# Kernel optimization log

Hardware: AMD Instinct MI355X
Metric: run time of the kernel (lower is better)

## Reference

```python
import jax, jax.numpy as jnp
import numpy as np

NUM_USER = 300000
NUM_ITEM = 200000
N = NUM_USER + NUM_ITEM
NNZ = 10000000
D = 64


def setup_inputs() -> dict:
    key = jax.random.key(0)
    k1, k2, k3, k4, k5, k6 = jax.random.split(key, 6)
    users_emb = jax.random.normal(k1, (NUM_USER, D), dtype=jnp.float32)
    items_emb = jax.random.normal(k2, (NUM_ITEM, D), dtype=jnp.float32)
    graph_vals = jax.random.uniform(k3, (NNZ,), dtype=jnp.float32)
    w = jax.random.normal(k4, (D, D), dtype=jnp.float32) * 0.1
    graph_rows = jax.random.randint(k5, (NNZ,), 0, N, dtype=jnp.int32)
    graph_cols = jax.random.randint(k6, (NNZ,), 0, N, dtype=jnp.int32)
    return {
        "users_emb": users_emb,
        "items_emb": items_emb,
        "graph_vals": graph_vals,
        "w": w,
        "graph_rows": graph_rows,
        "graph_cols": graph_cols,
    }


def reference(users_emb, items_emb, graph_vals, w, graph_rows, graph_cols):
    num_user = users_emb.shape[0]
    all_emb = jnp.concatenate([users_emb, items_emb], axis=0)  # [N, D]
    # sparse.mm(graph, all_emb): gather source rows, scale by edge value, scatter-add to dest rows
    msgs = graph_vals[:, None] * all_emb[graph_cols]  # [nnz, D]
    agg = jax.ops.segment_sum(msgs, graph_rows, num_segments=all_emb.shape[0])  # [N, D]
    out = agg @ w                      # non_linear dense transform
    out = jax.nn.leaky_relu(out, negative_slope=0.2)  # activation
    h_u2 = out[:num_user]
    h_i2 = out[num_user:]
    return (h_u2, h_i2)
```

## Files before the change

kernel.cpp:

```cpp
#include <hip/hip_runtime.h>
#include <hip/hip_bf16.h>

#define NUM_USER 300000
#define NUM_ITEM 200000
#define NTOT (NUM_USER + NUM_ITEM)
#define D 64
#define RPB 128
#define NB ((NTOT + RPB - 1) / RPB)
#define NBLK 256
#define ASTR 65
#define AW 8


__global__ __launch_bounds__(256) void hist_bucket(
    const int* __restrict__ rows, int* __restrict__ blockhist, int nnz)
{
    __shared__ int h[NB];
    for (int i = threadIdx.x; i < NB; i += 256) h[i] = 0;
    __syncthreads();
    int chunk = (nnz + NBLK - 1) / NBLK;
    int lo = blockIdx.x * chunk;
    int hi = min(lo + chunk, nnz);
    for (int e = lo + threadIdx.x; e < hi; e += 256)
        atomicAdd(&h[__builtin_nontemporal_load(&rows[e]) >> 7], 1);
    __syncthreads();
    for (int i = threadIdx.x; i < NB; i += 256)
        blockhist[blockIdx.x * NB + i] = h[i];
}


__global__ __launch_bounds__(256) void colscan(
    int* __restrict__ blockhist, int* __restrict__ coltotal)
{
    int kb = blockIdx.x * 256 + threadIdx.x;
    if (kb >= NB) return;
    int sum = 0;
    for (int b = 0; b < NBLK; b++) {
        int v = blockhist[b * NB + kb];
        blockhist[b * NB + kb] = sum;
        sum += v;
    }
    coltotal[kb] = sum;
}


__global__ __launch_bounds__(256) void bucketscan(
    const int* __restrict__ coltotal, int* __restrict__ bucketbase, int nnz)
{
    __shared__ int s[256];
    int t = threadIdx.x;
    int local[16];
    int sum = 0;
    #pragma unroll
    for (int i = 0; i < 16; i++) {
        int idx = t * 16 + i;
        int c = (idx < NB) ? coltotal[idx] : 0;
        local[i] = sum;
        sum += c;
    }
    s[t] = sum;
    __syncthreads();
    int v = sum;
    for (int off = 1; off < 256; off <<= 1) {
        int add = (t >= off) ? s[t - off] : 0;
        __syncthreads();
        s[t] += add;
        __syncthreads();
    }
    int base = s[t] - v;
    #pragma unroll
    for (int i = 0; i < 16; i++) {
        int idx = t * 16 + i;
        if (idx < NB) bucketbase[idx] = base + local[i];
    }
    if (t == 255) bucketbase[NB] = base + sum;
}


template<bool FAST>
__global__ __launch_bounds__(256) void scatter_bucket(
    const int* __restrict__ rows, const int* __restrict__ cols,
    const float* __restrict__ vals,
    const int* __restrict__ blockhist, const int* __restrict__ bucketbase,
    int* __restrict__ order, int2* __restrict__ rec2, int nnz)
{
    __shared__ int cur[NB];
    for (int i = threadIdx.x; i < NB; i += 256)
        cur[i] = blockhist[blockIdx.x * NB + i] + bucketbase[i];
    __syncthreads();
    int chunk = (nnz + NBLK - 1) / NBLK;
    int lo = blockIdx.x * chunk;
    int hi = min(lo + chunk, nnz);
    for (int e = lo + threadIdx.x; e < hi; e += 256) {
        int r = __builtin_nontemporal_load(&rows[e]);
        int pos = atomicAdd(&cur[r >> 7], 1);
        if (FAST) {
            int   c = __builtin_nontemporal_load(&cols[e]);
            float v = __builtin_nontemporal_load(&vals[e]);
            rec2[pos] = make_int2(((r & (RPB - 1)) << 19) | c,
                                  __float_as_int(v));
        } else {
            order[pos] = ((r & (RPB - 1)) << 24) | e;
        }
    }
}


__global__ __launch_bounds__(256) void rescatter2(
    const long long* __restrict__ rec2, const int* __restrict__ bucketbase,
    int* __restrict__ rowptr, long long* __restrict__ rec3)
{
    __shared__ int cnt[RPB];
    __shared__ int cur[RPB];
    __shared__ int s[256];
    int t = threadIdx.x;
    int kb = blockIdx.x;
    int row0 = kb * RPB;
    int start = bucketbase[kb], end = bucketbase[kb + 1];

    if (t < RPB) cnt[t] = 0;
    __syncthreads();
    for (int i = start + t; i < end; i += 256) {
        int key = (int)(rec2[i] & 0xffffffffLL);
        atomicAdd(&cnt[(key >> 19) & (RPB - 1)], 1);
    }
    __syncthreads();
    int v = (t < RPB) ? cnt[t] : 0;
    s[t] = v;
    __syncthreads();
    for (int off = 1; off < 256; off <<= 1) {
        int add = (t >= off) ? s[t - off] : 0;
        __syncthreads();
        s[t] += add;
        __syncthreads();
    }
    if (t < RPB) {
        int excl = s[t] - v;
        int p = start + excl;
        cur[t] = p;
        if (row0 + t <= NTOT) rowptr[row0 + t] = p;
    }
    __syncthreads();
    for (int i = start + t; i < end; i += 256) {
        long long rc = rec2[i];
        int key = (int)(rc & 0xffffffffLL);
        int lr  = (key >> 19) & (RPB - 1);
        int pos = atomicAdd(&cur[lr], 1);
        long long outrec = (rc & 0xffffffff00000000LL)
                         | (unsigned int)(key & 0x7FFFF);
        rec3[pos] = outrec;
    }
}


__global__ __launch_bounds__(256) void gather_rows(
    const float* __restrict__ users_emb, const float* __restrict__ items_emb,
    const long long* __restrict__ rec3, const int* __restrict__ rowptr,
    float* __restrict__ out, int n)
{
    int r = blockIdx.x * 4 + (threadIdx.x >> 6);
    if (r >= n) return;
    int lane = threadIdx.x & 63;
    int sub  = lane >> 4;
    int qi   = lane & 15;
    int k0 = rowptr[r];
    int k1 = rowptr[r + 1];
    float4 a0 = make_float4(0.f, 0.f, 0.f, 0.f);
    float4 a1 = make_float4(0.f, 0.f, 0.f, 0.f);
    #pragma unroll 2
    for (int g = k0; g < k1; g += 8) {
        int ka = g + sub;
        int kb = g + 4 + sub;
        long long rca = __builtin_nontemporal_load(&rec3[ka < k1 ? ka : k1 - 1]);
        long long rcb = __builtin_nontemporal_load(&rec3[kb < k1 ? kb : k1 - 1]);
        int   ca = (int)(rca & 0x7FFFFLL);
        int   cb = (int)(rcb & 0x7FFFFLL);
        float va = (ka < k1) ? __int_as_float((int)(rca >> 32)) : 0.f;
        float vb = (kb < k1) ? __int_as_float((int)(rcb >> 32)) : 0.f;
        const float* sa = (ca < NUM_USER)
            ? users_emb + (size_t)ca * D
            : items_emb + (size_t)(ca - NUM_USER) * D;
        const float* sb = (cb < NUM_USER)
            ? users_emb + (size_t)cb * D
            : items_emb + (size_t)(cb - NUM_USER) * D;
        float4 ea = *(const float4*)(sa + (qi << 2));
        float4 eb = *(const float4*)(sb + (qi << 2));
        a0.x = fmaf(va, ea.x, a0.x); a0.y = fmaf(va, ea.y, a0.y);
        a0.z = fmaf(va, ea.z, a0.z); a0.w = fmaf(va, ea.w, a0.w);
        a1.x = fmaf(vb, eb.x, a1.x); a1.y = fmaf(vb, eb.y, a1.y);
        a1.z = fmaf(vb, eb.z, a1.z); a1.w = fmaf(vb, eb.w, a1.w);
    }
    float4 a;
    a.x = a0.x + a1.x; a.y = a0.y + a1.y;
    a.z = a0.z + a1.z; a.w = a0.w + a1.w;
    a.x += __shfl_xor(a.x, 16); a.y += __shfl_xor(a.y, 16);
    a.z += __shfl_xor(a.z, 16); a.w += __shfl_xor(a.w, 16);
    a.x += __shfl_xor(a.x, 32); a.y += __shfl_xor(a.y, 32);
    a.z += __shfl_xor(a.z, 32); a.w += __shfl_xor(a.w, 32);
    if (sub == 0)
        *(float4*)(out + (size_t)r * D + (qi << 2)) = a;
}


template<bool FAST>
__global__ __launch_bounds__(512) void accum_kernel(
    const float* __restrict__ users_emb, const float* __restrict__ items_emb,
    const float* __restrict__ vals, const int* __restrict__ cols,
    const long long* __restrict__ rec2, const int* __restrict__ order,
    const int* __restrict__ bucketbase, float* __restrict__ out)
{
    __shared__ float acc[RPB * ASTR];
    int tid = threadIdx.x;
    for (int i = tid; i < RPB * ASTR; i += 512) acc[i] = 0.f;
    __syncthreads();

    int kb = blockIdx.x;
    int start = bucketbase[kb];
    int end   = bucketbase[kb + 1];
    int lane = tid & 63;
    int wid  = tid >> 6;
    int sub  = lane >> 4;
    int qi   = lane & 15;

    int span = end - start;
    int T = (span + (AW * 4 - 1)) / (AW * 4);
    int e0 = start + wid * 4 + sub;

    for (int it = 0; it < T; it++) {
        int e  = e0 + it * (AW * 4);
        int ec = max(start, min(e, end - 1));
        int ck; float v;
        if (FAST) {
            long long rc = __builtin_nontemporal_load(&rec2[ec]);
            ck = (int)(rc & 0xffffffffLL);
            v  = (e < end) ? __int_as_float((int)(rc >> 32)) : 0.f;
        } else {
            int rec  = __builtin_nontemporal_load(&order[ec]);
            int eid  = rec & 0xFFFFFF;
            int lrow = rec >> 24;
            ck = __builtin_nontemporal_load(&cols[eid]) | (lrow << 19);
            v  = (e < end) ? __builtin_nontemporal_load(&vals[eid]) : 0.f;
        }
        int cj = ck & 0x7FFFF;
        int lr = (ck >> 19) & (RPB - 1);
        const float* src = (cj < NUM_USER)
            ? users_emb + (size_t)cj * D
            : items_emb + (size_t)(cj - NUM_USER) * D;
        float4 e4 = *(const float4*)(src + (qi << 2));
        int ab = lr * ASTR + (qi << 2);
        atomicAdd(&acc[ab + 0], v * e4.x);
        atomicAdd(&acc[ab + 1], v * e4.y);
        atomicAdd(&acc[ab + 2], v * e4.z);
        atomicAdd(&acc[ab + 3], v * e4.w);
    }
    __syncthreads();

    size_t row0 = (size_t)kb * RPB;
    float4* o4 = (float4*)(out + row0 * D);
    for (int i = tid; i < RPB * (D / 4); i += 512) {
        int row = i >> 4, c4 = (i & 15) << 2;
        size_t grow = row0 + row;
        if (grow < NTOT) {
            float4 o;
            o.x = acc[row * ASTR + c4 + 0];
            o.y = acc[row * ASTR + c4 + 1];
            o.z = acc[row * ASTR + c4 + 2];
            o.w = acc[row * ASTR + c4 + 3];
            o4[i] = o;
        }
    }
}


__global__ __launch_bounds__(256) void rowgemm_kernel(
    float* __restrict__ out, const float* __restrict__ w, int n)
{
    __shared__ float ws[D * D];
    __shared__ float as[16 * D];
    int tid = threadIdx.x;

    const float4* w4 = (const float4*)w;
    float4* ws4 = (float4*)ws;
    #pragma unroll
    for (int i = 0; i < 4; i++) ws4[tid + i * 256] = w4[tid + i * 256];

    size_t row0 = (size_t)blockIdx.x * 16;
    ((float4*)as)[tid] = ((const float4*)(out + row0 * D))[tid];
    __syncthreads();

    int col  = tid & 63;
    int rsub = tid >> 6;
    float res[4];
    #pragma unroll
    for (int rr = 0; rr < 4; rr++) {
        int row = rr * 4 + rsub;
        float acc = 0.f;
        #pragma unroll
        for (int k = 0; k < D; k++) {
            acc = fmaf(as[row * D + k], ws[k * D + col], acc);
        }
        res[rr] = acc > 0.f ? acc : 0.2f * acc;
    }
    #pragma unroll
    for (int rr = 0; rr < 4; rr++) {
        int row = rr * 4 + rsub;
        out[(row0 + row) * D + col] = res[rr];
    }
}

extern "C" void kernel_launch(void* const* d_in, const int* in_sizes, int n_in,
                              void* d_out, int out_size, void* d_ws, size_t ws_size,
                              hipStream_t stream) {
    const float* users_emb = (const float*)d_in[0];
    const float* items_emb = (const float*)d_in[1];
    const float* vals      = (const float*)d_in[2];
    const float* w         = (const float*)d_in[3];
    const int*   rows      = (const int*)d_in[4];
    const int*   cols      = (const int*)d_in[5];
    float* out = (float*)d_out;

    int nnz = in_sizes[2];
    int n   = NTOT;

    char* ws = (char*)d_ws;
    int* blockhist  = (int*)(ws);
    int* coltotal   = (int*)(ws + (4ull << 20));
    int* bucketbase = (int*)(ws + (4ull << 20) + (64ull << 10));
    int* rowptr     = (int*)(ws + (6ull << 20));
    void* recbuf    = (void*)(ws + (8ull << 20));
    void* rec3buf   = (void*)(ws + (88ull << 20));

    bool fast  = ws_size >= (8ull << 20) + (size_t)nnz * 8ull;
    bool fast3 = ws_size >= (88ull << 20) + (size_t)nnz * 8ull;

    hist_bucket<<<NBLK, 256, 0, stream>>>(rows, blockhist, nnz);
    colscan<<<(NB + 255) / 256, 256, 0, stream>>>(blockhist, coltotal);
    bucketscan<<<1, 256, 0, stream>>>(coltotal, bucketbase, nnz);

    if (fast3) {
        scatter_bucket<true><<<NBLK, 256, 0, stream>>>(
            rows, cols, vals, blockhist, bucketbase,
            nullptr, (int2*)recbuf, nnz);
        rescatter2<<<NB, 256, 0, stream>>>(
            (const long long*)recbuf, bucketbase, rowptr, (long long*)rec3buf);
        gather_rows<<<(n + 3) / 4, 256, 0, stream>>>(
            users_emb, items_emb, (const long long*)rec3buf, rowptr, out, n);
    } else if (fast) {
        scatter_bucket<true><<<NBLK, 256, 0, stream>>>(
            rows, cols, vals, blockhist, bucketbase,
            nullptr, (int2*)recbuf, nnz);
        accum_kernel<true><<<NB, 512, 0, stream>>>(
            users_emb, items_emb, vals, cols,
            (const long long*)recbuf, nullptr, bucketbase, out);
    } else {
        scatter_bucket<false><<<NBLK, 256, 0, stream>>>(
            rows, cols, vals, blockhist, bucketbase,
            (int*)recbuf, nullptr, nnz);
        accum_kernel<false><<<NB, 512, 0, stream>>>(
            users_emb, items_emb, vals, cols,
            nullptr, (const int*)recbuf, bucketbase, out);
    }

    rowgemm_kernel<<<n / 16, 256, 0, stream>>>(out, w, n);
}
```

Measured before the change: 1.212 ms.

## Use more histogram/scatter blocks, compact workspace, widen gather unroll

Adds a new path that is taken when the workspace is large enough. It raises the block count for the histogram and bucket-scatter kernels from 256 to 1024 to increase parallelism, and it packs the workspace so rec3 reuses the blockhist region. The gather kernel now handles 16 edges per iteration with four independent accumulators, which puts more loads in flight. The trade-offs are a longer serial colscan over 1024 blocks, a larger blockhist, and higher register pressure in the gather kernel.

```diff
diff --git a/kernel.cpp b/kernel.cpp
--- a/kernel.cpp
+++ b/kernel.cpp
@@ -8,36 +8,37 @@
 #define RPB 128
 #define NB ((NTOT + RPB - 1) / RPB)
 #define NBLK 256
+#define NBLK2 1024
 #define ASTR 65
 #define AW 8
 
 
 __global__ __launch_bounds__(256) void hist_bucket(
-    const int* __restrict__ rows, int* __restrict__ blockhist, int nnz)
+    const int* __restrict__ rows, int* __restrict__ blockhist, int nnz, int nblk)
 {
     __shared__ int h[NB];
     for (int i = threadIdx.x; i < NB; i += 256) h[i] = 0;
     __syncthreads();
-    int chunk = (nnz + NBLK - 1) / NBLK;
+    int chunk = (nnz + nblk - 1) / nblk;
     int lo = blockIdx.x * chunk;
     int hi = min(lo + chunk, nnz);
     for (int e = lo + threadIdx.x; e < hi; e += 256)
         atomicAdd(&h[__builtin_nontemporal_load(&rows[e]) >> 7], 1);
     __syncthreads();
     for (int i = threadIdx.x; i < NB; i += 256)
-        blockhist[blockIdx.x * NB + i] = h[i];
+        blockhist[(size_t)blockIdx.x * NB + i] = h[i];
 }
 
 
 __global__ __launch_bounds__(256) void colscan(
-    int* __restrict__ blockhist, int* __restrict__ coltotal)
+    int* __restrict__ blockhist, int* __restrict__ coltotal, int nblk)
 {
     int kb = blockIdx.x * 256 + threadIdx.x;
     if (kb >= NB) return;
     int sum = 0;
-    for (int b = 0; b < NBLK; b++) {
-        int v = blockhist[b * NB + kb];
-        blockhist[b * NB + kb] = sum;
+    for (int b = 0; b < nblk; b++) {
+        int v = blockhist[(size_t)b * NB + kb];
+        blockhist[(size_t)b * NB + kb] = sum;
         sum += v;
     }
     coltotal[kb] = sum;
@@ -82,13 +83,13 @@
     const int* __restrict__ rows, const int* __restrict__ cols,
     const float* __restrict__ vals,
     const int* __restrict__ blockhist, const int* __restrict__ bucketbase,
-    int* __restrict__ order, int2* __restrict__ rec2, int nnz)
+    int* __restrict__ order, int2* __restrict__ rec2, int nnz, int nblk)
 {
     __shared__ int cur[NB];
     for (int i = threadIdx.x; i < NB; i += 256)
-        cur[i] = blockhist[blockIdx.x * NB + i] + bucketbase[i];
-    __syncthreads();
-    int chunk = (nnz + NBLK - 1) / NBLK;
+        cur[i] = blockhist[(size_t)blockIdx.x * NB + i] + bucketbase[i];
+    __syncthreads();
+    int chunk = (nnz + nblk - 1) / nblk;
     int lo = blockIdx.x * chunk;
     int hi = min(lo + chunk, nnz);
     for (int e = lo + threadIdx.x; e < hi; e += 256) {
@@ -167,32 +168,46 @@
     int k1 = rowptr[r + 1];
     float4 a0 = make_float4(0.f, 0.f, 0.f, 0.f);
     float4 a1 = make_float4(0.f, 0.f, 0.f, 0.f);
-    #pragma unroll 2
-    for (int g = k0; g < k1; g += 8) {
-        int ka = g + sub;
-        int kb = g + 4 + sub;
+    float4 a2 = make_float4(0.f, 0.f, 0.f, 0.f);
+    float4 a3 = make_float4(0.f, 0.f, 0.f, 0.f);
+    for (int g = k0; g < k1; g += 16) {
+        int ka = g + sub, kb = g + 4 + sub, kc = g + 8 + sub, kd = g + 12 + sub;
         long long rca = __builtin_nontemporal_load(&rec3[ka < k1 ? ka : k1 - 1]);
         long long rcb = __builtin_nontemporal_load(&rec3[kb < k1 ? kb : k1 - 1]);
-        int   ca = (int)(rca & 0x7FFFFLL);
-        int   cb = (int)(rcb & 0x7FFFFLL);
+        long long rcc = __builtin_nontemporal_load(&rec3[kc < k1 ? kc : k1 - 1]);
+        long long rcd = __builtin_nontemporal_load(&rec3[kd < k1 ? kd : k1 - 1]);
+        int ca = (int)(rca & 0x7FFFFLL), cb = (int)(rcb & 0x7FFFFLL);
+        int cc = (int)(rcc & 0x7FFFFLL), cd = (int)(rcd & 0x7FFFFLL);
         float va = (ka < k1) ? __int_as_float((int)(rca >> 32)) : 0.f;
         float vb = (kb < k1) ? __int_as_float((int)(rcb >> 32)) : 0.f;
-        const float* sa = (ca < NUM_USER)
-            ? users_emb + (size_t)ca * D
-            : items_emb + (size_t)(ca - NUM_USER) * D;
-        const float* sb = (cb < NUM_USER)
-            ? users_emb + (size_t)cb * D
-            : items_emb + (size_t)(cb - NUM_USER) * D;
+        float vc = (kc < k1) ? __int_as_float((int)(rcc >> 32)) : 0.f;
+        float vd = (kd < k1) ? __int_as_float((int)(rcd >> 32)) : 0.f;
+        const float* sa = (ca < NUM_USER) ? users_emb + (size_t)ca * D
+                                          : items_emb + (size_t)(ca - NUM_USER) * D;
+        const float* sb = (cb < NUM_USER) ? users_emb + (size_t)cb * D
+                                          : items_emb + (size_t)(cb - NUM_USER) * D;
+        const float* sc = (cc < NUM_USER) ? users_emb + (size_t)cc * D
+                                          : items_emb + (size_t)(cc - NUM_USER) * D;
+        const float* sd = (cd < NUM_USER) ? users_emb + (size_t)cd * D
+                                          : items_emb + (size_t)(cd - NUM_USER) * D;
         float4 ea = *(const float4*)(sa + (qi << 2));
         float4 eb = *(const float4*)(sb + (qi << 2));
+        float4 ec = *(const float4*)(sc + (qi << 2));
+        float4 ed = *(const float4*)(sd + (qi << 2));
         a0.x = fmaf(va, ea.x, a0.x); a0.y = fmaf(va, ea.y, a0.y);
         a0.z = fmaf(va, ea.z, a0.z); a0.w = fmaf(va, ea.w, a0.w);
         a1.x = fmaf(vb, eb.x, a1.x); a1.y = fmaf(vb, eb.y, a1.y);
         a1.z = fmaf(vb, eb.z, a1.z); a1.w = fmaf(vb, eb.w, a1.w);
+        a2.x = fmaf(vc, ec.x, a2.x); a2.y = fmaf(vc, ec.y, a2.y);
+        a2.z = fmaf(vc, ec.z, a2.z); a2.w = fmaf(vc, ec.w, a2.w);
+        a3.x = fmaf(vd, ed.x, a3.x); a3.y = fmaf(vd, ed.y, a3.y);
+        a3.z = fmaf(vd, ed.z, a3.z); a3.w = fmaf(vd, ed.w, a3.w);
     }
     float4 a;
-    a.x = a0.x + a1.x; a.y = a0.y + a1.y;
-    a.z = a0.z + a1.z; a.w = a0.w + a1.w;
+    a.x = (a0.x + a1.x) + (a2.x + a3.x);
+    a.y = (a0.y + a1.y) + (a2.y + a3.y);
+    a.z = (a0.z + a1.z) + (a2.z + a3.z);
+    a.w = (a0.w + a1.w) + (a2.w + a3.w);
     a.x += __shfl_xor(a.x, 16); a.y += __shfl_xor(a.y, 16);
     a.z += __shfl_xor(a.z, 16); a.w += __shfl_xor(a.w, 16);
     a.x += __shfl_xor(a.x, 32); a.y += __shfl_xor(a.y, 32);
@@ -321,8 +336,36 @@
 
     int nnz = in_sizes[2];
     int n   = NTOT;
-
     char* ws = (char*)d_ws;
+
+    size_t rec3Bytes = (size_t)nnz * 8ull;
+    size_t bhBytes   = (size_t)NBLK2 * NB * 4ull;
+    size_t offRec2   = rec3Bytes > bhBytes ? rec3Bytes : bhBytes;
+    size_t offMeta   = offRec2 + (size_t)nnz * 8ull;
+    size_t needP     = offMeta + (128ull << 10) + ((size_t)NTOT + 1) * 4ull;
+
+    if (ws_size >= needP) {
+        int* blockhist  = (int*)(ws);
+        long long* rec3 = (long long*)(ws);
+        int2* rec2      = (int2*)(ws + offRec2);
+        int* coltotal   = (int*)(ws + offMeta);
+        int* bucketbase = (int*)(ws + offMeta + (64ull << 10));
+        int* rowptr     = (int*)(ws + offMeta + (128ull << 10));
+
+        hist_bucket<<<NBLK2, 256, 0, stream>>>(rows, blockhist, nnz, NBLK2);
+        colscan<<<(NB + 255) / 256, 256, 0, stream>>>(blockhist, coltotal, NBLK2);
+        bucketscan<<<1, 256, 0, stream>>>(coltotal, bucketbase, nnz);
+        scatter_bucket<true><<<NBLK2, 256, 0, stream>>>(
+            rows, cols, vals, blockhist, bucketbase,
+            nullptr, rec2, nnz, NBLK2);
+        rescatter2<<<NB, 256, 0, stream>>>(
+            (const long long*)rec2, bucketbase, rowptr, rec3);
+        gather_rows<<<(n + 3) / 4, 256, 0, stream>>>(
+            users_emb, items_emb, (const long long*)rec3, rowptr, out, n);
+        rowgemm_kernel<<<n / 16, 256, 0, stream>>>(out, w, n);
+        return;
+    }
+
     int* blockhist  = (int*)(ws);
     int* coltotal   = (int*)(ws + (4ull << 20));
     int* bucketbase = (int*)(ws + (4ull << 20) + (64ull << 10));
@@ -333,14 +376,14 @@
     bool fast  = ws_size >= (8ull << 20) + (size_t)nnz * 8ull;
     bool fast3 = ws_size >= (88ull << 20) + (size_t)nnz * 8ull;
 
-    hist_bucket<<<NBLK, 256, 0, stream>>>(rows, blockhist, nnz);
-    colscan<<<(NB + 255) / 256, 256, 0, stream>>>(blockhist, coltotal);
+    hist_bucket<<<NBLK, 256, 0, stream>>>(rows, blockhist, nnz, NBLK);
+    colscan<<<(NB + 255) / 256, 256, 0, stream>>>(blockhist, coltotal, NBLK);
     bucketscan<<<1, 256, 0, stream>>>(coltotal, bucketbase, nnz);
 
     if (fast3) {
         scatter_bucket<true><<<NBLK, 256, 0, stream>>>(
             rows, cols, vals, blockhist, bucketbase,
-            nullptr, (int2*)recbuf, nnz);
+            nullptr, (int2*)recbuf, nnz, NBLK);
         rescatter2<<<NB, 256, 0, stream>>>(
             (const long long*)recbuf, bucketbase, rowptr, (long long*)rec3buf);
         gather_rows<<<(n + 3) / 4, 256, 0, stream>>>(
@@ -348,14 +391,14 @@
     } else if (fast) {
         scatter_bucket<true><<<NBLK, 256, 0, stream>>>(
             rows, cols, vals, blockhist, bucketbase,
-            nullptr, (int2*)recbuf, nnz);
+            nullptr, (int2*)recbuf, nnz, NBLK);
         accum_kernel<true><<<NB, 512, 0, stream>>>(
             users_emb, items_emb, vals, cols,
             (const long long*)recbuf, nullptr, bucketbase, out);
     } else {
         scatter_bucket<false><<<NBLK, 256, 0, stream>>>(
             rows, cols, vals, blockhist, bucketbase,
-            (int*)recbuf, nullptr, nnz);
+            (int*)recbuf, nullptr, nnz, NBLK);
         accum_kernel<false><<<NB, 512, 0, stream>>>(
             users_emb, items_emb, vals, cols,
             nullptr, (const int*)recbuf, bucketbase, out);
```

After: 1.352 ms. 11.5% more time.
